# Kernel optimization log

Measured on AMD Instinct MI355X. Metric: run time of the kernel, lower is better.

The kernel has to match this reference:

```python
import jax, jax.numpy as jnp
import numpy as np

N, D_IN, D_H, K, E = 100000, 128, 256, 16, 3200000


def setup_inputs() -> dict:
    key = jax.random.key(0)
    ks = jax.random.split(key, 6)
    x = jax.random.normal(ks[0], (N, D_IN), dtype=jnp.float32)
    edge_index = jax.random.randint(ks[1], (2, E), 0, N, dtype=jnp.int64)
    # Linear params (stored as [in, out] for x @ W + b)
    W1 = jax.random.normal(ks[2], (D_IN, D_H), dtype=jnp.float32) * 0.05
    b1 = jnp.zeros((D_H,), dtype=jnp.float32)
    W2 = jax.random.normal(ks[3], (D_H, K), dtype=jnp.float32) * 0.05
    b2 = jnp.zeros((K,), dtype=jnp.float32)
    return {"x": x, "edge_index": edge_index, "W1": W1, "b1": b1, "W2": W2, "b2": b2}


def reference(x, edge_index, W1, b1, W2, b2):
    # 2-layer MLP + row softmax -> soft cluster assignments C [N, K]
    h = jax.nn.relu(x @ W1 + b1)
    C = jax.nn.softmax(h @ W2 + b2, axis=1)
    # trace((C C^T)^T @ adj) == sum over edges (u,v) of C[u] . C[v]
    # (exact, incl. duplicate edges, since to_dense_adj scatter-adds 1 per edge)
    src, dst = edge_index[0], edge_index[1]
    edge_sum = jnp.sum(C[src] * C[dst])  # [E, K] gathered dot products, reduced
    num_edges = jnp.asarray(edge_index.shape[1], dtype=C.dtype)  # adj.sum()
    modularity_loss = -edge_sum / num_edges
    return (C, modularity_loss)
```

## Files before the change

### kernel.cpp

```cpp
#include <hip/hip_runtime.h>

#define N_NODES 100000
#define D_INF   128
#define D_HID   256
#define K_CL    16
#define N_TILES (N_NODES / 16)
#define N_EDGES 3200000
#define EDGE_BLOCKS (N_EDGES / 1024)

typedef __attribute__((ext_vector_type(8))) __bf16  bf16x8;
typedef __attribute__((ext_vector_type(8))) unsigned short u16x8;
typedef __attribute__((ext_vector_type(4))) float   f32x4;

__device__ __forceinline__ unsigned short f2bf(float f) {
    unsigned int u = __builtin_bit_cast(unsigned int, f);
    u += 0x7fffu + ((u >> 16) & 1u);
    return (unsigned short)(u >> 16);
}
__device__ __forceinline__ float bflo(unsigned int p) {
    return __builtin_bit_cast(float, p << 16);
}
__device__ __forceinline__ float bfhi(unsigned int p) {
    return __builtin_bit_cast(float, p & 0xffff0000u);
}

__global__ void prep_kernel(const float* __restrict__ W1,
                            const float* __restrict__ W2,
                            unsigned short* __restrict__ w1t,
                            unsigned short* __restrict__ w2t)
{
    const int i = blockIdx.x * 256 + threadIdx.x;
    if (i < D_INF * D_HID) {
        const int n = i >> 7, k = i & 127;
        w1t[i] = f2bf(W1[k * D_HID + n]);
    }
    if (i < D_HID * K_CL) {
        const int t = i >> 8, n = i & 255;
        w2t[i] = f2bf(W2[n * K_CL + t]);
    }
}

#define W1S 136
#define CHS 40

__global__ __launch_bounds__(256, 2) void mlp_kernel(
    const float* __restrict__ x, const unsigned short* __restrict__ W1T,
    const float* __restrict__ b1, const unsigned short* __restrict__ W2T,
    const float* __restrict__ b2, float* __restrict__ C,
    unsigned short* __restrict__ Cb)
{
    __shared__ unsigned short w1s[256 * W1S];
    __shared__ unsigned short chbuf[4][2][16 * CHS];
    __shared__ float b1s[D_HID];

    const int tid  = threadIdx.x;
    const int wv   = tid >> 6;
    const int lane = tid & 63;
    const int c    = lane & 15;
    const int q    = lane >> 4;

    #pragma unroll
    for (int it = 0; it < 16; ++it) {
        const int idx = it * 256 + tid;
        const int row = idx >> 4, ch = idx & 15;
        const uint4 v = ((const uint4*)W1T)[idx];
        *(uint4*)&w1s[row * W1S + ch * 8] = v;
    }
    if (tid < D_HID) b1s[tid] = b1[tid];

    bf16x8 w2f[8];
    #pragma unroll
    for (int kc2 = 0; kc2 < 8; ++kc2)
        w2f[kc2] = *(const bf16x8*)(W2T + (size_t)c * D_HID + kc2 * 32 + q * 8);
    const float b2v = b2[c];
    __syncthreads();

    unsigned short* const chA = &chbuf[wv][0][0];
    unsigned short* const chB = &chbuf[wv][1][0];

    const int wid     = blockIdx.x * 4 + wv;
    const int wstride = gridDim.x * 4;

    float4 xraw[8];
    {
        const float* xr = x + (size_t)(wid * 16 + c) * D_INF + q * 8;
        #pragma unroll
        for (int j = 0; j < 8; ++j)
            xraw[j] = *(const float4*)(xr + (j >> 1) * 32 + (j & 1) * 4);
    }

    for (int tile = wid; tile < N_TILES; tile += wstride) {
        const int m0 = tile * 16;

        const int nxt = tile + wstride;
        float4 xnxt[8];
        if (nxt < N_TILES) {
            const float* xr = x + (size_t)(nxt * 16 + c) * D_INF + q * 8;
            #pragma unroll
            for (int j = 0; j < 8; ++j)
                xnxt[j] = *(const float4*)(xr + (j >> 1) * 32 + (j & 1) * 4);
        }

        bf16x8 afr[4];
        #pragma unroll
        for (int kc = 0; kc < 4; ++kc) {
            const float4 xa = xraw[kc * 2], xb = xraw[kc * 2 + 1];
            u16x8 af;
            af[0] = f2bf(xa.x); af[1] = f2bf(xa.y); af[2] = f2bf(xa.z); af[3] = f2bf(xa.w);
            af[4] = f2bf(xb.x); af[5] = f2bf(xb.y); af[6] = f2bf(xb.z); af[7] = f2bf(xb.w);
            afr[kc] = __builtin_bit_cast(bf16x8, af);
        }

        f32x4 acc2 = (f32x4){0.f, 0.f, 0.f, 0.f};
        #pragma unroll
        for (int kc2 = 0; kc2 < 8; ++kc2) {
            unsigned short* const cb = (kc2 & 1) ? chB : chA;
            #pragma unroll
            for (int half = 0; half < 2; ++half) {
                const int nt = kc2 * 2 + half;
                f32x4 a1 = (f32x4){0.f, 0.f, 0.f, 0.f};
                #pragma unroll
                for (int kc = 0; kc < 4; ++kc) {
                    const bf16x8 bf =
                        *(const bf16x8*)&w1s[(nt * 16 + c) * W1S + kc * 32 + q * 8];
                    a1 = __builtin_amdgcn_mfma_f32_16x16x32_bf16(afr[kc], bf, a1, 0, 0, 0);
                }
                const float bv = b1s[nt * 16 + c];
                #pragma unroll
                for (int r = 0; r < 4; ++r)
                    cb[(4 * q + r) * CHS + half * 16 + c] =
                        f2bf(fmaxf(a1[r] + bv, 0.f));
            }
            const bf16x8 a2 = *(const bf16x8*)&cb[c * CHS + q * 8];
            acc2 = __builtin_amdgcn_mfma_f32_16x16x32_bf16(a2, w2f[kc2], acc2, 0, 0, 0);
        }

        #pragma unroll
        for (int r = 0; r < 4; ++r) {
            const float l = acc2[r] + b2v;
            float mx = l;
            mx = fmaxf(mx, __shfl_xor(mx, 1));
            mx = fmaxf(mx, __shfl_xor(mx, 2));
            mx = fmaxf(mx, __shfl_xor(mx, 4));
            mx = fmaxf(mx, __shfl_xor(mx, 8));
            const float e = __expf(l - mx);
            float sm = e;
            sm += __shfl_xor(sm, 1);
            sm += __shfl_xor(sm, 2);
            sm += __shfl_xor(sm, 4);
            sm += __shfl_xor(sm, 8);
            const float p = e / sm;
            const size_t o = (size_t)(m0 + 4 * q + r) * K_CL + c;
            C[o]  = p;
            Cb[o] = f2bf(p);
        }

        if (nxt < N_TILES) {
            #pragma unroll
            for (int j = 0; j < 8; ++j) xraw[j] = xnxt[j];
        }
    }
}

__global__ __launch_bounds__(256) void edge_kernel(
    const int* __restrict__ ei, const unsigned short* __restrict__ Cb,
    float* __restrict__ partials)
{
    __shared__ float red[4];
    const int tid  = threadIdx.x;
    const int lane = tid & 63;
    const int wv   = tid >> 6;
    const int base = (blockIdx.x * 4 + wv) * 256;

    int u[4], v[4];
    #pragma unroll
    for (int j = 0; j < 4; ++j) {
        u[j] = ei[base + j * 64 + lane];
        v[j] = ei[N_EDGES + base + j * 64 + lane];
    }

    const int half8 = (lane & 1) * 8;
    const int sl    = lane >> 1;

    float s = 0.f;
    #pragma unroll
    for (int g = 0; g < 8; ++g) {
        const int src = (g & 1) * 32 + sl;
        const int ue  = __shfl(u[g >> 1], src);
        const int ve  = __shfl(v[g >> 1], src);
        const uint4 a = *(const uint4*)(Cb + (size_t)ue * K_CL + half8);
        const uint4 b = *(const uint4*)(Cb + (size_t)ve * K_CL + half8);
        s = fmaf(bflo(a.x), bflo(b.x), s);
        s = fmaf(bfhi(a.x), bfhi(b.x), s);
        s = fmaf(bflo(a.y), bflo(b.y), s);
        s = fmaf(bfhi(a.y), bfhi(b.y), s);
        s = fmaf(bflo(a.z), bflo(b.z), s);
        s = fmaf(bfhi(a.z), bfhi(b.z), s);
        s = fmaf(bflo(a.w), bflo(b.w), s);
        s = fmaf(bfhi(a.w), bfhi(b.w), s);
    }
    s += __shfl_xor(s, 1);
    s += __shfl_xor(s, 2);
    s += __shfl_xor(s, 4);
    s += __shfl_xor(s, 8);
    s += __shfl_xor(s, 16);
    s += __shfl_xor(s, 32);
    if (lane == 0) red[wv] = s;
    __syncthreads();
    if (tid == 0) partials[blockIdx.x] = red[0] + red[1] + red[2] + red[3];
}

__global__ __launch_bounds__(256) void finalize_kernel(
    const float* __restrict__ partials, float* __restrict__ out)
{
    __shared__ float red[4];
    const int tid = threadIdx.x;
    float s = 0.f;
    for (int i = tid; i < EDGE_BLOCKS; i += 256) s += partials[i];
    s += __shfl_xor(s, 1);
    s += __shfl_xor(s, 2);
    s += __shfl_xor(s, 4);
    s += __shfl_xor(s, 8);
    s += __shfl_xor(s, 16);
    s += __shfl_xor(s, 32);
    if ((tid & 63) == 0) red[tid >> 6] = s;
    __syncthreads();
    if (tid == 0)
        out[(size_t)N_NODES * K_CL] =
            -(red[0] + red[1] + red[2] + red[3]) / (float)N_EDGES;
}

extern "C" void kernel_launch(void* const* d_in, const int* in_sizes, int n_in,
                              void* d_out, int out_size, void* d_ws, size_t ws_size,
                              hipStream_t stream) {
    const float* x  = (const float*)d_in[0];
    const int*   ei = (const int*)  d_in[1];
    const float* W1 = (const float*)d_in[2];
    const float* b1 = (const float*)d_in[3];
    const float* W2 = (const float*)d_in[4];
    const float* b2 = (const float*)d_in[5];
    float* out = (float*)d_out;

    unsigned short* w1t      = (unsigned short*)d_ws;
    unsigned short* w2t      = (unsigned short*)((char*)d_ws + 65536);
    unsigned short* Cb       = (unsigned short*)((char*)d_ws + 73760);
    float*          partials = (float*)((char*)d_ws + 3273760);

    prep_kernel<<<128, 256, 0, stream>>>(W1, W2, w1t, w2t);
    mlp_kernel<<<512, 256, 0, stream>>>(x, w1t, b1, w2t, b2, out, Cb);
    edge_kernel<<<EDGE_BLOCKS, 256, 0, stream>>>(ei, Cb, partials);
    finalize_kernel<<<1, 256, 0, stream>>>(partials, out);
}
```

Before: 154.8 us.

## Store cluster assignments as FP8 and gather one full row per lane in edge kernel

The MLP kernel now writes an FP8 copy of the softmax output instead of a bf16 copy, halving the size of the gathered table to 16 bytes per node. The edge kernel loads a whole 16-byte row per lane for each of its four edges, with no shuffles, and unpacks it with hardware fp8-to-f32 conversions before the dot products. Gather traffic and cache footprint for the random accesses both shrink. The cost is lower precision in the modularity sum, since FP8 e4m3 has far less mantissa than bf16, and a tolerance risk.

```diff
diff --git a/kernel.cpp b/kernel.cpp
--- a/kernel.cpp
+++ b/kernel.cpp
@@ -11,18 +11,14 @@
 typedef __attribute__((ext_vector_type(8))) __bf16  bf16x8;
 typedef __attribute__((ext_vector_type(8))) unsigned short u16x8;
 typedef __attribute__((ext_vector_type(4))) float   f32x4;
+typedef __attribute__((ext_vector_type(2))) float   f32x2;
+typedef __attribute__((ext_vector_type(4))) unsigned int u32x4;
 
 __device__ __forceinline__ unsigned short f2bf(float f) {
     unsigned int u = __builtin_bit_cast(unsigned int, f);
     u += 0x7fffu + ((u >> 16) & 1u);
     return (unsigned short)(u >> 16);
 }
-__device__ __forceinline__ float bflo(unsigned int p) {
-    return __builtin_bit_cast(float, p << 16);
-}
-__device__ __forceinline__ float bfhi(unsigned int p) {
-    return __builtin_bit_cast(float, p & 0xffff0000u);
-}
 
 __global__ void prep_kernel(const float* __restrict__ W1,
                             const float* __restrict__ W2,
@@ -47,7 +43,7 @@
     const float* __restrict__ x, const unsigned short* __restrict__ W1T,
     const float* __restrict__ b1, const unsigned short* __restrict__ W2T,
     const float* __restrict__ b2, float* __restrict__ C,
-    unsigned short* __restrict__ Cb)
+    unsigned char* __restrict__ C8)
 {
     __shared__ unsigned short w1s[256 * W1S];
     __shared__ unsigned short chbuf[4][2][16 * CHS];
@@ -152,7 +148,8 @@
             const float p = e / sm;
             const size_t o = (size_t)(m0 + 4 * q + r) * K_CL + c;
             C[o]  = p;
-            Cb[o] = f2bf(p);
+            C8[o] = (unsigned char)
+                (__builtin_amdgcn_cvt_pk_fp8_f32(p, p, 0, false) & 0xff);
         }
 
         if (nxt < N_TILES) {
@@ -162,8 +159,8 @@
     }
 }
 
-__global__ __launch_bounds__(256) void edge_kernel(
-    const int* __restrict__ ei, const unsigned short* __restrict__ Cb,
+__global__ __launch_bounds__(256, 5) void edge_kernel(
+    const int* __restrict__ ei, const unsigned char* __restrict__ C8,
     float* __restrict__ partials)
 {
     __shared__ float red[4];
@@ -179,26 +176,33 @@
         v[j] = ei[N_EDGES + base + j * 64 + lane];
     }
 
-    const int half8 = (lane & 1) * 8;
-    const int sl    = lane >> 1;
-
-    float s = 0.f;
-    #pragma unroll
-    for (int g = 0; g < 8; ++g) {
-        const int src = (g & 1) * 32 + sl;
-        const int ue  = __shfl(u[g >> 1], src);
-        const int ve  = __shfl(v[g >> 1], src);
-        const uint4 a = *(const uint4*)(Cb + (size_t)ue * K_CL + half8);
-        const uint4 b = *(const uint4*)(Cb + (size_t)ve * K_CL + half8);
-        s = fmaf(bflo(a.x), bflo(b.x), s);
-        s = fmaf(bfhi(a.x), bfhi(b.x), s);
-        s = fmaf(bflo(a.y), bflo(b.y), s);
-        s = fmaf(bfhi(a.y), bfhi(b.y), s);
-        s = fmaf(bflo(a.z), bflo(b.z), s);
-        s = fmaf(bfhi(a.z), bfhi(b.z), s);
-        s = fmaf(bflo(a.w), bflo(b.w), s);
-        s = fmaf(bfhi(a.w), bfhi(b.w), s);
-    }
+    u32x4 A[4], B[4];
+    #pragma unroll
+    for (int j = 0; j < 4; ++j) {
+        A[j] = *(const u32x4*)(C8 + (size_t)u[j] * 16);
+        B[j] = *(const u32x4*)(C8 + (size_t)v[j] * 16);
+    }
+
+    float s0 = 0.f, s1 = 0.f, s2 = 0.f, s3 = 0.f;
+    #pragma unroll
+    for (int j = 0; j < 4; ++j) {
+        float t = 0.f;
+        #pragma unroll
+        for (int d = 0; d < 4; ++d) {
+            const f32x2 a0 = __builtin_amdgcn_cvt_pk_f32_fp8(A[j][d], false);
+            const f32x2 a1 = __builtin_amdgcn_cvt_pk_f32_fp8(A[j][d], true);
+            const f32x2 b0 = __builtin_amdgcn_cvt_pk_f32_fp8(B[j][d], false);
+            const f32x2 b1 = __builtin_amdgcn_cvt_pk_f32_fp8(B[j][d], true);
+            t = fmaf(a0[0], b0[0], t);
+            t = fmaf(a0[1], b0[1], t);
+            t = fmaf(a1[0], b1[0], t);
+            t = fmaf(a1[1], b1[1], t);
+        }
+        if (j == 0) s0 = t; else if (j == 1) s1 = t;
+        else if (j == 2) s2 = t; else s3 = t;
+    }
+    float s = (s0 + s1) + (s2 + s3);
+
     s += __shfl_xor(s, 1);
     s += __shfl_xor(s, 2);
     s += __shfl_xor(s, 4);
@@ -243,11 +247,11 @@
 
     unsigned short* w1t      = (unsigned short*)d_ws;
     unsigned short* w2t      = (unsigned short*)((char*)d_ws + 65536);
-    unsigned short* Cb       = (unsigned short*)((char*)d_ws + 73760);
-    float*          partials = (float*)((char*)d_ws + 3273760);
+    unsigned char*  C8       = (unsigned char*)((char*)d_ws + 73760);
+    float*          partials = (float*)((char*)d_ws + 1673760);
 
     prep_kernel<<<128, 256, 0, stream>>>(W1, W2, w1t, w2t);
-    mlp_kernel<<<512, 256, 0, stream>>>(x, w1t, b1, w2t, b2, out, Cb);
-    edge_kernel<<<EDGE_BLOCKS, 256, 0, stream>>>(ei, Cb, partials);
+    mlp_kernel<<<512, 256, 0, stream>>>(x, w1t, b1, w2t, b2, out, C8);
+    edge_kernel<<<EDGE_BLOCKS, 256, 0, stream>>>(ei, C8, partials);
     finalize_kernel<<<1, 256, 0, stream>>>(partials, out);
 }
```

New measurement: 152.8 us, median of 2. About the same (-1.3%).
